# Optimization experiments

Measured on AMD Instinct MI355X. Metric: run time of the kernel, lower is better.

## Reference

```python
import jax, jax.numpy as jnp
import numpy as np


def setup_inputs() -> dict:
    key = jax.random.key(0)
    ks = iter(jax.random.split(key, 100))
    V3, Vm, K, E3, Em = 100000, 25000, 128, 800000, 200000
    c_in, c3, cm, c_out = 16, 128, 256, 21
    rn = lambda *s: jax.random.normal(next(ks), s, dtype=jnp.float32)
    ru = lambda *s: jax.random.uniform(next(ks), s, dtype=jnp.float32)
    ri = lambda hi, *s: jax.random.randint(next(ks), s, 0, hi)
    d = {}
    d['x_in'] = rn(1, V3, c_in)
    d['mass_3'] = ru(1, V3)
    d['evals_3'] = ru(1, K)
    d['evecs_3'] = rn(1, V3, K) * 0.01
    d['gX3_idx'] = ri(V3, E3, 2)
    d['gX3_val'] = rn(E3) * 0.05
    d['gY3_idx'] = ri(V3, E3, 2)
    d['gY3_val'] = rn(E3) * 0.05
    d['mass_m'] = ru(1, Vm)
    d['evals_m'] = ru(1, K)
    d['evecs_m'] = rn(1, Vm, K) * 0.01
    d['gXm_idx'] = ri(Vm, Em, 2)
    d['gXm_val'] = rn(Em) * 0.05
    d['gYm_idx'] = ri(Vm, Em, 2)
    d['gYm_val'] = rn(Em) * 0.05
    d['traces34'] = ri(Vm, V3)
    d['in_w'] = rn(c_in, c3) * 0.05
    d['in_b'] = rn(c3) * 0.05
    d['widen_w'] = rn(c3, cm) * 0.05
    d['widen_b'] = rn(cm) * 0.05
    d['narrow_w'] = rn(cm, c3) * 0.05
    d['narrow_b'] = rn(c3) * 0.05
    d['halve_w'] = rn(2 * c3, c3) * 0.05
    d['halve_b'] = rn(c3) * 0.05
    d['out_w'] = rn(c3, c_out) * 0.05
    d['out_b'] = rn(c_out) * 0.05
    for pre, C in (('enc', c3), ('mid', cm), ('dec', c3)):
        d[pre + '_dt'] = ru(2, C)
        d[pre + '_Are'] = rn(2, C, C) * 0.05
        d[pre + '_Aim'] = rn(2, C, C) * 0.05
        d[pre + '_w0'] = rn(2, 3 * C, C) * 0.05
        d[pre + '_b0'] = rn(2, C) * 0.05
        d[pre + '_w1'] = rn(2, C, C) * 0.05
        d[pre + '_b1'] = rn(2, C) * 0.05
        d[pre + '_w2'] = rn(2, C, C) * 0.05
        d[pre + '_b2'] = rn(2, C) * 0.05
    return d


def _spmm(idx, val, x, n):
    # sparse COO (n x n) @ x ; rows = idx[:,0], cols = idx[:,1]
    return jax.ops.segment_sum(val[:, None] * x[idx[:, 1]], idx[:, 0], num_segments=n)


def _block(x, mass, evals, evecs, gxi, gxv, gyi, gyv, dt, Are, Aim, w0, b0, w1, b1, w2, b2):
    # DiffusionNetBlock: spectral diffusion + rotated gradient features + MiniMLP + residual
    V = x.shape[1]
    x_spec = jnp.einsum('bvk,bvc->bkc', evecs, x * mass[..., None])          # to_basis
    coef = jnp.exp(-evals[..., None] * jnp.maximum(dt, 1e-8)[None, None, :])  # (B,K,C)
    xd = jnp.einsum('bvk,bkc->bvc', evecs, coef * x_spec)                     # from_basis
    gX = _spmm(gxi, gxv, xd[0], V)[None]                                      # (B,V,C)
    gY = _spmm(gyi, gyv, xd[0], V)[None]
    Br = gX @ Are - gY @ Aim                                                  # complex linear, with rotations
    Bi = gY @ Are + gX @ Aim
    gf = jnp.tanh(gX * Br + gY * Bi)                                          # inner product -> tanh
    h = jnp.concatenate([x, xd, gf], axis=-1)                                 # (B,V,3C)
    h = jax.nn.relu(h @ w0 + b0)
    h = jax.nn.relu(h @ w1 + b1)
    return (h @ w2 + b2) + x


def reference(x_in, mass_3, evals_3, evecs_3, gX3_idx, gX3_val, gY3_idx, gY3_val,
              mass_m, evals_m, evecs_m, gXm_idx, gXm_val, gYm_idx, gYm_val, traces34,
              in_w, in_b, enc_dt, enc_Are, enc_Aim, enc_w0, enc_b0, enc_w1, enc_b1, enc_w2, enc_b2,
              widen_w, widen_b, mid_dt, mid_Are, mid_Aim, mid_w0, mid_b0, mid_w1, mid_b1, mid_w2, mid_b2,
              narrow_w, narrow_b, halve_w, halve_b,
              dec_dt, dec_Are, dec_Aim, dec_w0, dec_b0, dec_w1, dec_b1, dec_w2, dec_b2,
              out_w, out_b):
    Vm = mass_m.shape[1]
    sl = lambda arrs, i: tuple(a[i] for a in arrs)
    enc_p = (enc_dt, enc_Are, enc_Aim, enc_w0, enc_b0, enc_w1, enc_b1, enc_w2, enc_b2)
    mid_p = (mid_dt, mid_Are, mid_Aim, mid_w0, mid_b0, mid_w1, mid_b1, mid_w2, mid_b2)
    dec_p = (dec_dt, dec_Are, dec_Aim, dec_w0, dec_b0, dec_w1, dec_b1, dec_w2, dec_b2)

    x3 = jax.nn.relu(x_in @ in_w + in_b)
    for i in range(enc_dt.shape[0]):
        x3 = _block(x3, mass_3, evals_3, evecs_3, gX3_idx, gX3_val, gY3_idx, gY3_val, *sl(enc_p, i))
    # scatter-max pooling fine -> coarse
    xm = jax.ops.segment_max(x3[0], traces34, num_segments=Vm)
    xm = jnp.where(jnp.isneginf(xm), 0.0, xm)[None]
    xm = jax.nn.relu(xm @ widen_w + widen_b)
    for i in range(mid_dt.shape[0]):
        xm = _block(xm, mass_m, evals_m, evecs_m, gXm_idx, gXm_val, gYm_idx, gYm_val, *sl(mid_p, i))
    # gather unpooling coarse -> fine
    y3 = xm[:, traces34, :]
    y3 = jax.nn.relu(y3 @ narrow_w + narrow_b)
    y3 = jnp.concatenate([y3, x3], axis=-1)
    y3 = jax.nn.relu(y3 @ halve_w + halve_b)
    for i in range(dec_dt.shape[0]):
        y3 = _block(y3, mass_3, evals_3, evecs_3, gX3_idx, gX3_val, gY3_idx, gY3_val, *sl(dec_p, i))
    return y3 @ out_w + out_b
```

## Files before the change

### kernel.cpp

```cpp
#include <hip/hip_runtime.h>
#include <cstdint>
#include <cstddef>

static constexpr int V3   = 100000;
static constexpr int VM   = 25000;
static constexpr int KE   = 128;
static constexpr int E3   = 800000;
static constexpr int EM   = 200000;
static constexpr int C3   = 128;
static constexpr int CMID = 256;

typedef unsigned short u16;
typedef unsigned int   u32;
using short8v = __attribute__((ext_vector_type(8))) short;
using f32x4   = __attribute__((ext_vector_type(4))) float;
using f32x16  = __attribute__((ext_vector_type(16))) float;

#define DEVI __device__ __forceinline__
DEVI float4 ld4(const float* p){ return *(const float4*)p; }
DEVI void   st4(float* p, float4 v){ *(float4*)p = v; }
DEVI float  bf2f(u16 u){ return __uint_as_float(((u32)u) << 16); }
DEVI u16    f2bf(float f){
  u32 u = __float_as_uint(f);
  u += 0x7FFFu + ((u >> 16) & 1u);
  return (u16)(u >> 16);
}
DEVI u32 pk2(float a, float b){ return (u32)f2bf(a) | ((u32)f2bf(b) << 16); }
DEVI short8v as8(uint4 v){ union { uint4 u; short8v s; } c; c.u = v; return c.s; }
DEVI int lofs(int row, int oct){ return row * 40 + ((oct ^ ((row >> 3) & 3)) << 3); }

static inline int cdiv(int a, int b){ return (a + b - 1) / b; }

template<bool RELU, bool RES, bool GATHER, bool OBF16>
__global__ __launch_bounds__(256)
void k_mgemm(const void* __restrict__ A0, int aty0, int K0,
             const u16* __restrict__ wt0, int wl0, int wo0,
             const void* __restrict__ A1, int aty1, int K1,
             const u16* __restrict__ wt1, int wl1, int wo1,
             const void* __restrict__ A2, int aty2, int K2,
             const u16* __restrict__ wt2, int wl2, int wo2,
             const int* __restrict__ gidx,
             const float* __restrict__ bias, const float* __restrict__ res,
             void* __restrict__ OUT, u16* __restrict__ OUTB, int CO, int V)
{
  __shared__ __align__(16) u16 As[64 * 40];
  __shared__ __align__(16) u16 Ws[128 * 40];

  const int tid  = threadIdx.x;
  const int wave = tid >> 6, lane = tid & 63;
  const int vbase = blockIdx.x * 64;
  const int ncol0 = blockIdx.y * 128;
  const int KT = K0 + K1 + K2;

  f32x4 acc[8];
  #pragma unroll
  for (int n = 0; n < 8; n++) { acc[n][0]=0.f; acc[n][1]=0.f; acc[n][2]=0.f; acc[n][3]=0.f; }

  const int ar = tid >> 2, ac = tid & 3;
  const int arow = vbase + ar;
  int grow0 = arow;
  if (GATHER && arow < V) grow0 = gidx[arow];

  for (int kt = 0; kt < KT; kt += 32) {
    {
      int kg = kt + ac * 8;
      uint4 aw = make_uint4(0,0,0,0);
      if (arow < V && kg < KT) {
        const void* src; int aty, koff, sK; bool s0;
        if (kg < K0)            { src=A0; aty=aty0; koff=0;     sK=K0; s0=true;  }
        else if (kg < K0 + K1)  { src=A1; aty=aty1; koff=K0;    sK=K1; s0=false; }
        else                    { src=A2; aty=aty2; koff=K0+K1; sK=K2; s0=false; }
        int row = (GATHER && s0) ? grow0 : arow;
        int kl = kg - koff;
        if (aty) {
          aw = *(const uint4*)((const u16*)src + (size_t)row * sK + kl);
        } else {
          const float* fp = (const float*)src + (size_t)row * sK + kl;
          float4 x = ld4(fp), y = ld4(fp + 4);
          aw = make_uint4(pk2(x.x,x.y), pk2(x.z,x.w), pk2(y.x,y.y), pk2(y.z,y.w));
        }
      }
      *(uint4*)&As[ar * 40 + ac * 8] = aw;
    }
    #pragma unroll
    for (int i = 0; i < 2; i++) {
      int col = tid & 127;
      int c = (tid >> 7) + 2 * i;
      int kg = kt + c * 8;
      uint4 ww = make_uint4(0,0,0,0);
      if (kg < KT) {
        const u16* wt; int koff, wl, wo;
        if (kg < K0)           { wt=wt0; koff=0;     wl=wl0; wo=wo0; }
        else if (kg < K0+K1)   { wt=wt1; koff=K0;    wl=wl1; wo=wo1; }
        else                   { wt=wt2; koff=K0+K1; wl=wl2; wo=wo2; }
        ww = *(const uint4*)(wt + (size_t)(ncol0 + col) * wl + wo + (kg - koff));
      }
      *(uint4*)&Ws[col * 40 + c * 8] = ww;
    }
    __syncthreads();
    {
      const int mrow = (wave << 4) + (lane & 15);
      const int kc = lane >> 4;
      short8v a = *(const short8v*)(const void*)&As[mrow * 40 + kc * 8];
      #pragma unroll
      for (int n = 0; n < 8; n++) {
        short8v b = *(const short8v*)(const void*)&Ws[(n * 16 + (lane & 15)) * 40 + kc * 8];
        acc[n] = __builtin_amdgcn_mfma_f32_16x16x32_bf16(a, b, acc[n], 0, 0, 0);
      }
    }
    __syncthreads();
  }

  const int q4 = (lane >> 4) * 4, colb = lane & 15;
  #pragma unroll
  for (int n = 0; n < 8; n++) {
    int gcol = ncol0 + n * 16 + colb;
    float bv = bias ? bias[gcol] : 0.f;
    #pragma unroll
    for (int q = 0; q < 4; q++) {
      int grow = vbase + (wave << 4) + q4 + q;
      if (grow >= V) continue;
      float o = acc[n][q] + bv;
      size_t idx = (size_t)grow * CO + gcol;
      if (RES) o += res[idx];
      if (RELU) o = fmaxf(o, 0.f);
      if (OBF16) ((u16*)OUT)[idx] = f2bf(o);
      else {
        ((float*)OUT)[idx] = o;
        if (OUTB) OUTB[idx] = f2bf(o);
      }
    }
  }
}

__global__ __launch_bounds__(256)
void k_mlp3(const u16* __restrict__ A0, const u16* __restrict__ A1,
            const u16* __restrict__ A2,
            const u16* __restrict__ w0t,
            const u16* __restrict__ w1t, const u16* __restrict__ w2t,
            const float* __restrict__ b0, const float* __restrict__ b1,
            const float* __restrict__ b2,
            float* __restrict__ XM, u16* __restrict__ SHB, int V)
{
  __shared__ __align__(16) u16 As[64 * 40];
  __shared__ __align__(16) u16 Ws[128 * 40];
  __shared__ __align__(16) u16 Hs[4][64 * 40];

  const int tid  = threadIdx.x;
  const int wave = tid >> 6, lane = tid & 63;
  const int vbase = blockIdx.x * 64;
  const int ar = tid >> 2, ac = tid & 3;
  const int arow = vbase + ar;
  const bool rok = arow < V;
  const int mrow = (wave << 4) + (lane & 15);
  const int kc = lane >> 4;
  const int q4 = (lane >> 4) * 4, colb = lane & 15;
  const int wcol = tid & 127, wc = tid >> 7;

  float xres[8][4];
  #pragma unroll
  for (int n = 0; n < 8; n++)
    #pragma unroll
    for (int q = 0; q < 4; q++) {
      int grow = vbase + (wave << 4) + q4 + q;
      xres[n][q] = (grow < V) ? XM[(size_t)grow * C3 + n * 16 + colb] : 0.f;
    }

  f32x4 acc[8];
  auto zacc = [&]{
    #pragma unroll
    for (int n = 0; n < 8; n++) { acc[n][0]=0.f; acc[n][1]=0.f; acc[n][2]=0.f; acc[n][3]=0.f; }
  };
  auto hwrite = [&](const float* b){
    #pragma unroll
    for (int n = 0; n < 8; n++) {
      int c = n * 16 + colb;
      float bv = b[c];
      #pragma unroll
      for (int q = 0; q < 4; q++) {
        int row = (wave << 4) + q4 + q;
        Hs[c >> 5][lofs(row, (c >> 3) & 3) + (c & 7)] = f2bf(fmaxf(acc[n][q] + bv, 0.f));
      }
    }
  };
  auto mfma_tile = [&](const u16* a8){
    short8v a = *(const short8v*)(const void*)a8;
    #pragma unroll
    for (int n = 0; n < 8; n++) {
      short8v b = *(const short8v*)(const void*)&Ws[(n * 16 + (lane & 15)) * 40 + kc * 8];
      acc[n] = __builtin_amdgcn_mfma_f32_16x16x32_bf16(a, b, acc[n], 0, 0, 0);
    }
  };
  auto fA = [&](int kg) -> uint4 {
    const u16* src = (kg < 128) ? A0 : (kg < 256) ? A1 : A2;
    uint4 r = make_uint4(0,0,0,0);
    if (rok) r = *(const uint4*)(src + (size_t)arow * 128 + (kg & 127));
    return r;
  };
  auto fW = [&](const u16* wt, int ld, int kg) -> uint4 {
    return *(const uint4*)(wt + (size_t)wcol * ld + kg);
  };

  zacc();
  uint4 pa  = fA(ac * 8);
  uint4 pw0 = fW(w0t, 384, wc * 8);
  uint4 pw1 = fW(w0t, 384, (wc + 2) * 8);
  for (int kt = 0; kt < 384; kt += 32) {
    __syncthreads();
    *(uint4*)&As[ar * 40 + ac * 8] = pa;
    *(uint4*)&Ws[wcol * 40 + wc * 8] = pw0;
    *(uint4*)&Ws[wcol * 40 + (wc + 2) * 8] = pw1;
    __syncthreads();
    int kn = kt + 32;
    if (kn < 384) {
      pa  = fA(kn + ac * 8);
      pw0 = fW(w0t, 384, kn + wc * 8);
      pw1 = fW(w0t, 384, kn + (wc + 2) * 8);
    } else {
      pw0 = fW(w1t, 128, wc * 8);
      pw1 = fW(w1t, 128, (wc + 2) * 8);
    }
    mfma_tile(&As[mrow * 40 + kc * 8]);
  }
  hwrite(b0);
  zacc();
  for (int kt = 0; kt < 128; kt += 32) {
    __syncthreads();
    *(uint4*)&Ws[wcol * 40 + wc * 8] = pw0;
    *(uint4*)&Ws[wcol * 40 + (wc + 2) * 8] = pw1;
    __syncthreads();
    int kn = kt + 32;
    if (kn < 128) {
      pw0 = fW(w1t, 128, kn + wc * 8);
      pw1 = fW(w1t, 128, kn + (wc + 2) * 8);
    } else {
      pw0 = fW(w2t, 128, wc * 8);
      pw1 = fW(w2t, 128, (wc + 2) * 8);
    }
    mfma_tile(&Hs[kt >> 5][lofs(mrow, kc)]);
  }
  hwrite(b1);
  zacc();
  for (int kt = 0; kt < 128; kt += 32) {
    __syncthreads();
    *(uint4*)&Ws[wcol * 40 + wc * 8] = pw0;
    *(uint4*)&Ws[wcol * 40 + (wc + 2) * 8] = pw1;
    __syncthreads();
    int kn = kt + 32;
    if (kn < 128) {
      pw0 = fW(w2t, 128, kn + wc * 8);
      pw1 = fW(w2t, 128, kn + (wc + 2) * 8);
    }
    mfma_tile(&Hs[kt >> 5][lofs(mrow, kc)]);
  }
  #pragma unroll
  for (int n = 0; n < 8; n++) {
    int gcol = n * 16 + colb;
    float bv = b2[gcol];
    #pragma unroll
    for (int q = 0; q < 4; q++) {
      int grow = vbase + (wave << 4) + q4 + q;
      if (grow >= V) continue;
      size_t idx = (size_t)grow * C3 + gcol;
      float o = acc[n][q] + bv + xres[n][q];
      XM[idx] = o;
      SHB[idx] = f2bf(o);
    }
  }
}

__global__ __launch_bounds__(256)
void k_mgate_reg(const u16* __restrict__ GEX, const u16* __restrict__ GEY,
                 const u16* __restrict__ pS, const u16* __restrict__ pR,
                 const u16* __restrict__ pI,
                 u16* __restrict__ GF, int CO, int V)
{
  const int lane = threadIdx.x & 63;
  const int wave = threadIdx.x >> 6;
  const int rbase = blockIdx.x * 128 + wave * 32;
  const int arow = rbase + (lane & 31);
  const int koff = (lane >> 5) * 8;
  const bool rok = arow < V;

  uint4 ax[8], ay[8], an[8];
  #pragma unroll
  for (int kt = 0; kt < 8; kt++) {
    uint4 zx = make_uint4(0,0,0,0), zy = make_uint4(0,0,0,0);
    if (rok) {
      zx = *(const uint4*)(GEX + (size_t)arow * KE + kt * 16 + koff);
      zy = *(const uint4*)(GEY + (size_t)arow * KE + kt * 16 + koff);
    }
    ax[kt] = zx; ay[kt] = zy;
    an[kt] = make_uint4(zy.x ^ 0x80008000u, zy.y ^ 0x80008000u,
                        zy.z ^ 0x80008000u, zy.w ^ 0x80008000u);
  }

  const int ngr = CO >> 5;
  for (int g = 0; g < ngr; g++) {
    f32x16 gx, gy, br, bi;
    #pragma unroll
    for (int r = 0; r < 16; r++) { gx[r]=0.f; gy[r]=0.f; br[r]=0.f; bi[r]=0.f; }
    #pragma unroll
    for (int kt = 0; kt < 8; kt++) {
      size_t bo = ((size_t)(g * 8 + kt) * 64 + lane) * 8;
      short8v bs  = *(const short8v*)(const void*)(pS + bo);
      short8v brv = *(const short8v*)(const void*)(pR + bo);
      short8v biv = *(const short8v*)(const void*)(pI + bo);
      short8v axv = as8(ax[kt]), ayv = as8(ay[kt]), anv = as8(an[kt]);
      gx = __builtin_amdgcn_mfma_f32_32x32x16_bf16(axv, bs,  gx, 0, 0, 0);
      gy = __builtin_amdgcn_mfma_f32_32x32x16_bf16(ayv, bs,  gy, 0, 0, 0);
      br = __builtin_amdgcn_mfma_f32_32x32x16_bf16(axv, brv, br, 0, 0, 0);
      br = __builtin_amdgcn_mfma_f32_32x32x16_bf16(anv, biv, br, 0, 0, 0);
      bi = __builtin_amdgcn_mfma_f32_32x32x16_bf16(axv, biv, bi, 0, 0, 0);
      bi = __builtin_amdgcn_mfma_f32_32x32x16_bf16(ayv, brv, bi, 0, 0, 0);
    }
    const int col = g * 32 + (lane & 31);
    const int rhi = 4 * (lane >> 5);
    #pragma unroll
    for (int r = 0; r < 16; r++) {
      int row = rbase + (r & 3) + 8 * (r >> 2) + rhi;
      if (row < V) {
        float o = tanhf(gx[r] * br[r] + gy[r] * bi[r]);
        GF[(size_t)row * CO + col] = f2bf(o);
      }
    }
  }
}

__global__ __launch_bounds__(256)
void k_specmm(const u16* __restrict__ E, const u16* __restrict__ X,
              const float* __restrict__ mass, float* __restrict__ SPEC,
              int C, int V, int CH)
{
  __shared__ __align__(16) u16 As[64 * 40];
  __shared__ __align__(16) u16 Bs[128 * 40];

  const int tid = threadIdx.x;
  const int wave = tid >> 6, lane = tid & 63;
  const int m0 = blockIdx.y * 64;
  const int n0 = blockIdx.z * 128;
  const int vs = blockIdx.x * CH;
  const int ve = min(V, vs + CH);

  f32x4 acc[8];
  #pragma unroll
  for (int n = 0; n < 8; n++) { acc[n][0]=0.f; acc[n][1]=0.f; acc[n][2]=0.f; acc[n][3]=0.f; }

  const int am = tid & 63, ac = tid >> 6;
  const int bcol = tid & 127, bc0 = (tid >> 7) * 2;

  u16 ea[8]; float fb0[8], fb1[8], fm0[8], fm1[8];
  auto loadA = [&](int kt) {
    #pragma unroll
    for (int j = 0; j < 8; j++) {
      int v = kt + ac * 8 + j;
      ea[j] = (v < ve) ? E[(size_t)v * KE + m0 + am] : (u16)0;
    }
  };
  auto loadB = [&](int kt) {
    #pragma unroll
    for (int j = 0; j < 8; j++) {
      int v0 = kt + bc0 * 8 + j, v1 = v0 + 8;
      fb0[j] = (v0 < ve) ? bf2f(X[(size_t)v0 * C + n0 + bcol]) : 0.f;
      fm0[j] = (v0 < ve) ? mass[v0] : 0.f;
      fb1[j] = (v1 < ve) ? bf2f(X[(size_t)v1 * C + n0 + bcol]) : 0.f;
      fm1[j] = (v1 < ve) ? mass[v1] : 0.f;
    }
  };
  loadA(vs); loadB(vs);

  for (int kt = vs; kt < ve; kt += 32) {
    __syncthreads();
    *(uint4*)&As[lofs(am, ac)] = make_uint4(
        (u32)ea[0] | ((u32)ea[1] << 16), (u32)ea[2] | ((u32)ea[3] << 16),
        (u32)ea[4] | ((u32)ea[5] << 16), (u32)ea[6] | ((u32)ea[7] << 16));
    float t0[8], t1[8];
    #pragma unroll
    for (int j = 0; j < 8; j++) { t0[j] = fb0[j]*fm0[j]; t1[j] = fb1[j]*fm1[j]; }
    *(uint4*)&Bs[lofs(bcol, bc0)] = make_uint4(
        pk2(t0[0],t0[1]), pk2(t0[2],t0[3]), pk2(t0[4],t0[5]), pk2(t0[6],t0[7]));
    *(uint4*)&Bs[lofs(bcol, bc0 + 1)] = make_uint4(
        pk2(t1[0],t1[1]), pk2(t1[2],t1[3]), pk2(t1[4],t1[5]), pk2(t1[6],t1[7]));
    __syncthreads();
    if (kt + 32 < ve) { loadA(kt + 32); loadB(kt + 32); }
    const int kc = lane >> 4, ml = lane & 15;
    short8v a = *(const short8v*)(const void*)&As[lofs(wave * 16 + ml, kc)];
    #pragma unroll
    for (int n = 0; n < 8; n++) {
      short8v b = *(const short8v*)(const void*)&Bs[lofs(n * 16 + ml, kc)];
      acc[n] = __builtin_amdgcn_mfma_f32_16x16x32_bf16(a, b, acc[n], 0, 0, 0);
    }
  }

  const int q4 = (lane >> 4) * 4, colb = lane & 15;
  #pragma unroll
  for (int n = 0; n < 8; n++) {
    int col = n0 + n * 16 + colb;
    #pragma unroll
    for (int q = 0; q < 4; q++) {
      int row = m0 + wave * 16 + q4 + q;
      unsafeAtomicAdd(&SPEC[(size_t)row * C + col], acc[n][q]);
    }
  }
}

template<int C>
__global__ void k_smallprep(const float* __restrict__ SPEC, const float* __restrict__ evals,
                            const float* __restrict__ dt, const float* __restrict__ Are,
                            const float* __restrict__ Aim, const float* __restrict__ w0,
                            u16* __restrict__ pS, u16* __restrict__ pR,
                            u16* __restrict__ pI, u16* __restrict__ SWt)
{
  __shared__ float sld[C];
  const int k = blockIdx.x;
  const int c = threadIdx.x;
  const float ev = evals[k];
  float s = expf(-ev * fmaxf(dt[c], 1e-8f)) * SPEC[(size_t)k * C + c];
  sld[c] = s;
  const size_t pidx = ((size_t)((c >> 5) * 8 + (k >> 4)) * 64
                       + (c & 31) + ((k >> 3) & 1) * 32) * 8 + (k & 7);
  pS[pidx] = f2bf(s);
  __syncthreads();
  float tr = 0.f, ti = 0.f, sw = 0.f;
  for (int j = 0; j < C; j++) {
    float sj = sld[j];
    tr = fmaf(sj, Are[(size_t)j * C + c], tr);
    ti = fmaf(sj, Aim[(size_t)j * C + c], ti);
    sw = fmaf(sj, w0[(size_t)(C + j) * C + c], sw);
  }
  pR[pidx] = f2bf(tr);
  pI[pidx] = f2bf(ti);
  SWt[(size_t)c * 128 + k] = f2bf(sw);
}

__global__ void k_asmw0(const u16* __restrict__ w0t_, const u16* __restrict__ swt_,
                        u16* __restrict__ o_) {
  int col = blockIdx.x, t = threadIdx.x;
  o_[(size_t)col * 384 + t]       = w0t_[(size_t)col * 384 + t];
  o_[(size_t)col * 384 + 128 + t] = w0t_[(size_t)col * 384 + 256 + t];
  o_[(size_t)col * 384 + 256 + t] = swt_[(size_t)col * 128 + t];
}

__global__ void k_prepw(const float* __restrict__ W, u16* __restrict__ WT, int K, int N) {
  size_t zoff = (size_t)blockIdx.z * K * N;
  int i = blockIdx.x * 256 + threadIdx.x;
  if (i < K * N) {
    int k = i / N, n = i % N;
    WT[zoff + (size_t)n * K + k] = f2bf(W[zoff + i]);
  }
}

__global__ void k_cvt(const float* __restrict__ in, u16* __restrict__ out, int n) {
  int i = (blockIdx.x * 256 + threadIdx.x) * 4;
  if (i < n) {
    float4 v = ld4(in + i);
    ushort4 o; o.x = f2bf(v.x); o.y = f2bf(v.y); o.z = f2bf(v.z); o.w = f2bf(v.w);
    *(ushort4*)(out + i) = o;
  }
}

__global__ void k_hist(const int* __restrict__ idx, int* __restrict__ deg, int E) {
  int e = blockIdx.x * 256 + threadIdx.x;
  if (e < E) atomicAdd(&deg[idx[2 * e]], 1);
}
__global__ void k_scan1(const int* __restrict__ deg, int* __restrict__ excl,
                        int* __restrict__ bsum, int V) {
  __shared__ int sd[256];
  int t = threadIdx.x;
  int i = blockIdx.x * 256 + t;
  int v = (i < V) ? deg[i] : 0;
  sd[t] = v;
  __syncthreads();
  for (int off = 1; off < 256; off <<= 1) {
    int add = (t >= off) ? sd[t - off] : 0;
    __syncthreads();
    sd[t] += add;
    __syncthreads();
  }
  if (i < V) excl[i] = sd[t] - v;
  if (t == 255) bsum[blockIdx.x] = sd[255];
}
__global__ void k_scan2(int* __restrict__ bsum, int nb, int* __restrict__ rowptr, int V) {
  __shared__ int sd[512];
  int t = threadIdx.x;
  int v = (t < nb) ? bsum[t] : 0;
  sd[t] = v;
  __syncthreads();
  for (int off = 1; off < 512; off <<= 1) {
    int add = (t >= off) ? sd[t - off] : 0;
    __syncthreads();
    sd[t] += add;
    __syncthreads();
  }
  if (t < nb) bsum[t] = sd[t] - v;
  if (t == 0) rowptr[V] = sd[511];
}
__global__ void k_scan3(const int* __restrict__ excl, const int* __restrict__ bsum,
                        int* __restrict__ rowptr, int V) {
  int i = blockIdx.x * 256 + threadIdx.x;
  if (i < V) rowptr[i] = excl[i] + bsum[i >> 8];
}
__global__ void k_scatter(const int* __restrict__ idx, const float* __restrict__ val,
                          const int* __restrict__ rowptr, int* __restrict__ cur,
                          int* __restrict__ ecol, float* __restrict__ eval, int E) {
  int e = blockIdx.x * 256 + threadIdx.x;
  if (e < E) {
    int d = idx[2 * e];
    int p = rowptr[d] + atomicAdd(&cur[d], 1);
    ecol[p] = idx[2 * e + 1];
    eval[p] = val[e];
  }
}
__global__ __launch_bounds__(256)
void k_spmm_csr(const int* __restrict__ rowptr, const int* __restrict__ ecol,
                const float* __restrict__ eval, const u16* __restrict__ E,
                u16* __restrict__ GE, int V) {
  int r = blockIdx.x * 8 + (threadIdx.x >> 5);
  int lane = threadIdx.x & 31;
  if (r >= V) return;
  int j1 = rowptr[r + 1];
  float4 a = make_float4(0.f,0.f,0.f,0.f);
  for (int j = rowptr[r]; j < j1; j++) {
    int c = ecol[j];
    float v = eval[j];
    ushort4 x = *(const ushort4*)(E + (size_t)c * KE + lane * 4);
    a.x = fmaf(v, bf2f(x.x), a.x); a.y = fmaf(v, bf2f(x.y), a.y);
    a.z = fmaf(v, bf2f(x.z), a.z); a.w = fmaf(v, bf2f(x.w), a.w);
  }
  ushort4 o;
  o.x = f2bf(a.x); o.y = f2bf(a.y); o.z = f2bf(a.z); o.w = f2bf(a.w);
  *(ushort4*)(GE + (size_t)r * KE + lane * 4) = o;
}

__global__ void k_segmax_init(unsigned* __restrict__ u, int n) {
  int i = blockIdx.x * 256 + threadIdx.x;
  if (i < n) u[i] = 0x007FFFFFu;
}
__global__ void k_segmax_scatter(const u16* __restrict__ X, const int* __restrict__ tr,
                                 unsigned* __restrict__ u) {
  int i = blockIdx.x * 256 + threadIdx.x;
  if (i >= V3 * C3) return;
  int v = i >> 7, c = i & 127;
  unsigned b = ((unsigned)X[i]) << 16;
  unsigned m = (b & 0x80000000u) ? ~b : (b | 0x80000000u);
  atomicMax(&u[((size_t)tr[v] << 7) + c], m);
}
__global__ void k_segmax_decode(const unsigned* __restrict__ u, u16* __restrict__ out, int n) {
  int i = blockIdx.x * 256 + threadIdx.x;
  if (i < n) {
    unsigned m = u[i];
    unsigned b = 0;
    if (m != 0x007FFFFFu)
      b = (m & 0x80000000u) ? (m & 0x7FFFFFFFu) : ~m;
    out[i] = (u16)(b >> 16);
  }
}

__global__ __launch_bounds__(256)
void k_outproj(const float* __restrict__ Y, const float* __restrict__ W,
               const float* __restrict__ B, float* __restrict__ OUT, int V) {
  __shared__ float Wl[128][22];
  __shared__ float ys[8][128];
  const int tid = threadIdx.x;
  for (int f = tid; f < 128 * 21; f += 256) Wl[f / 21][f % 21] = W[f];
  {
    int r = tid >> 5, cc = (tid & 31) * 4;
    int v = blockIdx.x * 8 + r;
    float4 yv = make_float4(0.f,0.f,0.f,0.f);
    if (v < V) yv = ld4(Y + (size_t)v * C3 + cc);
    st4(&ys[r][cc], yv);
  }
  __syncthreads();
  int r = tid >> 5, c = tid & 31;
  int v = blockIdx.x * 8 + r;
  if (v < V && c < 21) {
    float acc = B[c];
    #pragma unroll 8
    for (int k = 0; k < 128; k++) acc = fmaf(ys[r][k], Wl[k][c], acc);
    OUT[(size_t)v * 21 + c] = acc;
  }
}

extern "C" void kernel_launch(void* const* d_in, const int* in_sizes, int n_in,
                              void* d_out, int out_size, void* d_ws, size_t ws_size,
                              hipStream_t stream)
{
  (void)in_sizes; (void)n_in; (void)out_size;
  const float* x_in    = (const float*)d_in[0];
  const float* mass3   = (const float*)d_in[1];
  const float* evals3  = (const float*)d_in[2];
  const float* evecs3  = (const float*)d_in[3];
  const int*   gX3i    = (const int*)d_in[4];
  const float* gX3v    = (const float*)d_in[5];
  const int*   gY3i    = (const int*)d_in[6];
  const float* gY3v    = (const float*)d_in[7];
  const float* massm   = (const float*)d_in[8];
  const float* evalsm  = (const float*)d_in[9];
  const float* evecsm  = (const float*)d_in[10];
  const int*   gXmi    = (const int*)d_in[11];
  const float* gXmv    = (const float*)d_in[12];
  const int*   gYmi    = (const int*)d_in[13];
  const float* gYmv    = (const float*)d_in[14];
  const int*   tr34    = (const int*)d_in[15];
  const float* in_w    = (const float*)d_in[16];
  const float* in_b    = (const float*)d_in[17];
  const float* widen_w = (const float*)d_in[18];
  const float* widen_b = (const float*)d_in[19];
  const float* narrow_w= (const float*)d_in[20];
  const float* narrow_b= (const float*)d_in[21];
  const float* halve_w = (const float*)d_in[22];
  const float* halve_b = (const float*)d_in[23];
  const float* out_w   = (const float*)d_in[24];
  const float* out_b   = (const float*)d_in[25];
  const float* enc_p[9]; const float* mid_p[9]; const float* dec_p[9];
  for (int i = 0; i < 9; i++) {
    enc_p[i] = (const float*)d_in[26 + i];
    mid_p[i] = (const float*)d_in[35 + i];
    dec_p[i] = (const float*)d_in[44 + i];
  }

  char* ws = (char*)d_ws;
  size_t off = 0;
  float* XM  = (float*)(ws + off); off += (size_t)V3 * C3 * 4;
  u16* SHB   = (u16*)(ws + off);   off += (size_t)V3 * C3 * 2;
  u16* GEX3  = (u16*)(ws + off);   off += (size_t)V3 * KE * 2;
  u16* GEY3  = (u16*)(ws + off);   off += (size_t)V3 * KE * 2;
  u16* GEXm  = (u16*)(ws + off);   off += (size_t)VM * KE * 2;
  u16* GEYm  = (u16*)(ws + off);   off += (size_t)VM * KE * 2;
  u16* BSCR  = (u16*)(ws + off);   off += (size_t)V3 * C3 * 2;
  char* E3R  = (char*)(ws + off);  off += (size_t)V3 * KE * 2;
  u16* Embf  = (u16*)(ws + off);   off += (size_t)VM * KE * 2;
  u16* SHM   = (u16*)(ws + off);   off += (size_t)VM * CMID * 2;
  float* spec= (float*)(ws + off); off += 131072;
  u16* pS  = (u16*)(ws + off); off += 65536;
  u16* pR  = (u16*)(ws + off); off += 65536;
  u16* pI  = (u16*)(ws + off); off += 65536;
  u16* SWt = (u16*)(ws + off); off += 65536;
  u16* wT  = (u16*)(ws + off); off += 2400000;
  const size_t NEED = off;
  if (ws_size < NEED) return;

  u16*   E3bf = (u16*)E3R;
  float* M0   = (float*)E3R;
  int*   rowptr = (int*)BSCR;
  int*   deg    = (int*)((char*)BSCR + 400128);
  int*   ecol   = (int*)((char*)BSCR + 800256);
  float* evalv  = (float*)((char*)BSCR + 4000256);
  int*   bsum   = (int*)((char*)BSCR + 7200256);
  unsigned* xm_u  = (unsigned*)BSCR;
  u16*      xm_dec= (u16*)((char*)BSCR + 12800000);
  u16* BSCR0 = BSCR;
  u16* BSCR1 = BSCR + (size_t)VM * CMID;

  u16* in_wt    = wT + 0;
  u16* widen_t  = wT + 2048;
  u16* narrow_t = wT + 34816;
  u16* halve_t  = wT + 67584;
  u16* enc_w0t  = wT + 100352;
  u16* enc_w1t  = wT + 198656;
  u16* enc_w2t  = wT + 231424;
  u16* mid_w0t  = wT + 264192;
  u16* mid_w1t  = wT + 657408;
  u16* mid_w2t  = wT + 788480;
  u16* dec_w0t  = wT + 919552;
  u16* dec_w1t  = wT + 1017856;
  u16* dec_w2t  = wT + 1050624;
  u16* wCmb     = wT + 1083392;

  auto prepw = [&](const float* W, u16* WT, int K, int N, int z) {
    k_prepw<<<dim3(cdiv(K * N, 256), 1, z), 256, 0, stream>>>(W, WT, K, N);
  };
  prepw(in_w, in_wt, 16, 128, 1);
  prepw(widen_w, widen_t, 128, 256, 1);
  prepw(narrow_w, narrow_t, 256, 128, 1);
  prepw(halve_w, halve_t, 256, 128, 1);
  prepw(enc_p[3], enc_w0t, 384, 128, 2);
  prepw(enc_p[5], enc_w1t, 128, 128, 2);
  prepw(enc_p[7], enc_w2t, 128, 128, 2);
  prepw(mid_p[3], mid_w0t, 768, 256, 2);
  prepw(mid_p[5], mid_w1t, 256, 256, 2);
  prepw(mid_p[7], mid_w2t, 256, 256, 2);
  prepw(dec_p[3], dec_w0t, 384, 128, 2);
  prepw(dec_p[5], dec_w1t, 128, 128, 2);
  prepw(dec_p[7], dec_w2t, 128, 128, 2);

  k_cvt<<<cdiv(V3 * KE / 4, 256), 256, 0, stream>>>(evecs3, E3bf, V3 * KE);
  k_cvt<<<cdiv(VM * KE / 4, 256), 256, 0, stream>>>(evecsm, Embf, VM * KE);

  auto build_ge = [&](const int* idx, const float* val, int E_, int V_,
                      const u16* Ebf, u16* GE) {
    hipMemsetAsync(deg, 0, (size_t)V_ * 4, stream);
    k_hist<<<cdiv(E_, 256), 256, 0, stream>>>(idx, deg, E_);
    int nb = cdiv(V_, 256);
    k_scan1<<<nb, 256, 0, stream>>>(deg, ecol, bsum, V_);
    k_scan2<<<1, 512, 0, stream>>>(bsum, nb, rowptr, V_);
    k_scan3<<<nb, 256, 0, stream>>>(ecol, bsum, rowptr, V_);
    hipMemsetAsync(deg, 0, (size_t)V_ * 4, stream);
    k_scatter<<<cdiv(E_, 256), 256, 0, stream>>>(idx, val, rowptr, deg, ecol, evalv, E_);
    k_spmm_csr<<<cdiv(V_, 8), 256, 0, stream>>>(rowptr, ecol, evalv, Ebf, GE, V_);
  };
  build_ge(gX3i, gX3v, E3, V3, E3bf, GEX3);
  build_ge(gY3i, gY3v, E3, V3, E3bf, GEY3);
  build_ge(gXmi, gXmv, EM, VM, Embf, GEXm);
  build_ge(gYmi, gYmv, EM, VM, Embf, GEYm);

  const int G3 = cdiv(V3, 64);
  const int GM = cdiv(VM, 64);

  auto launch_block3 = [&](const float* p[9],
                           const u16* w0t, const u16* w1t, const u16* w2t, int i) {
    const float* dt  = p[0] + (size_t)i * C3;
    const float* Are = p[1] + (size_t)i * C3 * C3;
    const float* Aim = p[2] + (size_t)i * C3 * C3;
    const float* w0  = p[3] + (size_t)i * 3 * C3 * C3;
    const float* b0  = p[4] + (size_t)i * C3;
    const float* b1  = p[6] + (size_t)i * C3;
    const float* b2  = p[8] + (size_t)i * C3;
    const u16* w0ti = w0t + (size_t)i * 3 * C3 * C3;
    const u16* w1ti = w1t + (size_t)i * C3 * C3;
    const u16* w2ti = w2t + (size_t)i * C3 * C3;
    hipMemsetAsync(spec, 0, (size_t)KE * C3 * 4, stream);
    k_specmm<<<dim3(cdiv(V3, 256), 2, 1), 256, 0, stream>>>(E3bf, SHB, mass3, spec, C3, V3, 256);
    k_smallprep<C3><<<KE, C3, 0, stream>>>(spec, evals3, dt, Are, Aim, w0, pS, pR, pI, SWt);
    k_mgate_reg<<<cdiv(V3, 128), 256, 0, stream>>>(GEX3, GEY3, pS, pR, pI, BSCR, C3, V3);
    k_asmw0<<<128, 128, 0, stream>>>(w0ti, SWt, wCmb);
    k_mlp3<<<G3, 256, 0, stream>>>(SHB, BSCR, E3bf, wCmb, w1ti, w2ti,
                                   b0, b1, b2, XM, SHB, V3);
  };

  auto run_blockm = [&](const float* p[9],
                        const u16* w0t, const u16* w1t, const u16* w2t, int i) {
    const float* dt  = p[0] + (size_t)i * CMID;
    const float* Are = p[1] + (size_t)i * CMID * CMID;
    const float* Aim = p[2] + (size_t)i * CMID * CMID;
    const float* w0  = p[3] + (size_t)i * 3 * CMID * CMID;
    const float* b0  = p[4] + (size_t)i * CMID;
    const float* b1  = p[6] + (size_t)i * CMID;
    const float* b2  = p[8] + (size_t)i * CMID;
    const u16* w0ti = w0t + (size_t)i * 3 * CMID * CMID;
    const u16* w1ti = w1t + (size_t)i * CMID * CMID;
    const u16* w2ti = w2t + (size_t)i * CMID * CMID;
    hipMemsetAsync(spec, 0, (size_t)KE * CMID * 4, stream);
    k_specmm<<<dim3(cdiv(VM, 128), 2, 2), 256, 0, stream>>>(Embf, SHM, massm, spec, CMID, VM, 128);
    k_smallprep<CMID><<<KE, CMID, 0, stream>>>(spec, evalsm, dt, Are, Aim, w0, pS, pR, pI, SWt);
    k_mgate_reg<<<cdiv(VM, 128), 256, 0, stream>>>(GEXm, GEYm, pS, pR, pI, BSCR0, CMID, VM);
    k_mgemm<true,false,false,true><<<dim3(GM, 2), 256, 0, stream>>>(
        SHM, 1, CMID, w0ti, 3*CMID, 0,
        BSCR0, 1, CMID, w0ti, 3*CMID, 2*CMID,
        Embf, 1, KE, SWt, 128, 0,
        nullptr, b0, nullptr, BSCR1, nullptr, CMID, VM);
    k_mgemm<true,false,false,true><<<dim3(GM, 2), 256, 0, stream>>>(
        BSCR1, 1, CMID, w1ti, CMID, 0,
        nullptr,0,0,nullptr,0,0, nullptr,0,0,nullptr,0,0,
        nullptr, b1, nullptr, BSCR0, nullptr, CMID, VM);
    k_mgemm<false,true,false,false><<<dim3(GM, 2), 256, 0, stream>>>(
        BSCR0, 1, CMID, w2ti, CMID, 0,
        nullptr,0,0,nullptr,0,0, nullptr,0,0,nullptr,0,0,
        nullptr, b2, M0, M0, SHM, CMID, VM);
  };

  k_mgemm<true,false,false,false><<<dim3(G3, 1), 256, 0, stream>>>(
      x_in, 0, 16, in_wt, 16, 0,
      nullptr,0,0,nullptr,0,0, nullptr,0,0,nullptr,0,0,
      nullptr, in_b, nullptr, XM, SHB, C3, V3);
  launch_block3(enc_p, enc_w0t, enc_w1t, enc_w2t, 0);
  launch_block3(enc_p, enc_w0t, enc_w1t, enc_w2t, 1);

  k_segmax_init<<<cdiv(VM * C3, 256), 256, 0, stream>>>(xm_u, VM * C3);
  k_segmax_scatter<<<cdiv(V3 * C3, 256), 256, 0, stream>>>(SHB, tr34, xm_u);
  k_segmax_decode<<<cdiv(VM * C3, 256), 256, 0, stream>>>(xm_u, xm_dec, VM * C3);
  k_mgemm<true,false,false,false><<<dim3(GM, 2), 256, 0, stream>>>(
      xm_dec, 1, C3, widen_t, C3, 0,
      nullptr,0,0,nullptr,0,0, nullptr,0,0,nullptr,0,0,
      nullptr, widen_b, nullptr, M0, SHM, CMID, VM);
  run_blockm(mid_p, mid_w0t, mid_w1t, mid_w2t, 0);
  run_blockm(mid_p, mid_w0t, mid_w1t, mid_w2t, 1);

  k_mgemm<true,false,true,true><<<dim3(G3, 1), 256, 0, stream>>>(
      SHM, 1, CMID, narrow_t, CMID, 0,
      nullptr,0,0,nullptr,0,0, nullptr,0,0,nullptr,0,0,
      tr34, narrow_b, nullptr, BSCR, nullptr, C3, V3);
  k_mgemm<true,false,false,false><<<dim3(G3, 1), 256, 0, stream>>>(
      BSCR, 1, C3, halve_t, 2*C3, 0,
      SHB, 1, C3, halve_t, 2*C3, C3,
      nullptr,0,0,nullptr,0,0,
      nullptr, halve_b, nullptr, XM, SHB, C3, V3);

  k_cvt<<<cdiv(V3 * KE / 4, 256), 256, 0, stream>>>(evecs3, E3bf, V3 * KE);
  launch_block3(dec_p, dec_w0t, dec_w1t, dec_w2t, 0);
  launch_block3(dec_p, dec_w0t, dec_w1t, dec_w2t, 1);

  k_outproj<<<cdiv(V3, 8), 256, 0, stream>>>(XM, out_w, out_b, (float*)d_out, V3);
}
```

Before: 2.005 ms.

## Pre-pack MLP weights into MFMA fragment order and drop LDS staging

```diff
diff --git a/kernel.cpp b/kernel.cpp
--- a/kernel.cpp
+++ b/kernel.cpp
@@ -134,37 +134,24 @@
 }
 
 __global__ __launch_bounds__(256)
-void k_mlp3(const u16* __restrict__ A0, const u16* __restrict__ A1,
-            const u16* __restrict__ A2,
-            const u16* __restrict__ w0t,
-            const u16* __restrict__ w1t, const u16* __restrict__ w2t,
-            const float* __restrict__ b0, const float* __restrict__ b1,
-            const float* __restrict__ b2,
-            float* __restrict__ XM, u16* __restrict__ SHB, int V)
+void k_mlp3r(const u16* __restrict__ A0, const u16* __restrict__ A1,
+             const u16* __restrict__ A2,
+             const u16* __restrict__ w0p,
+             const u16* __restrict__ w1p, const u16* __restrict__ w2p,
+             const float* __restrict__ b0, const float* __restrict__ b1,
+             const float* __restrict__ b2,
+             float* __restrict__ XM, u16* __restrict__ SHB, int V)
 {
-  __shared__ __align__(16) u16 As[64 * 40];
-  __shared__ __align__(16) u16 Ws[128 * 40];
   __shared__ __align__(16) u16 Hs[4][64 * 40];
 
   const int tid  = threadIdx.x;
   const int wave = tid >> 6, lane = tid & 63;
   const int vbase = blockIdx.x * 64;
-  const int ar = tid >> 2, ac = tid & 3;
-  const int arow = vbase + ar;
+  const int colb = lane & 15;
+  const int q4 = (lane >> 4) * 4;
+  const int kq = (lane >> 4) * 8;
+  const int arow = vbase + wave * 16 + colb;
   const bool rok = arow < V;
-  const int mrow = (wave << 4) + (lane & 15);
-  const int kc = lane >> 4;
-  const int q4 = (lane >> 4) * 4, colb = lane & 15;
-  const int wcol = tid & 127, wc = tid >> 7;
-
-  float xres[8][4];
-  #pragma unroll
-  for (int n = 0; n < 8; n++)
-    #pragma unroll
-    for (int q = 0; q < 4; q++) {
-      int grow = vbase + (wave << 4) + q4 + q;
-      xres[n][q] = (grow < V) ? XM[(size_t)grow * C3 + n * 16 + colb] : 0.f;
-    }
 
   f32x4 acc[8];
   auto zacc = [&]{
@@ -183,75 +170,41 @@
       }
     }
   };
-  auto mfma_tile = [&](const u16* a8){
-    short8v a = *(const short8v*)(const void*)a8;
+
+  zacc();
+  #pragma unroll
+  for (int kc = 0; kc < 12; kc++) {
+    int kg = kc * 32 + kq;
+    const u16* src = (kg < 128) ? A0 : (kg < 256) ? A1 : A2;
+    short8v a = as8(make_uint4(0,0,0,0));
+    if (rok) a = *(const short8v*)(const void*)(src + (size_t)arow * 128 + (kg & 127));
     #pragma unroll
     for (int n = 0; n < 8; n++) {
-      short8v b = *(const short8v*)(const void*)&Ws[(n * 16 + (lane & 15)) * 40 + kc * 8];
+      short8v b = *(const short8v*)(const void*)(w0p + ((size_t)(n * 12 + kc) * 64 + lane) * 8);
       acc[n] = __builtin_amdgcn_mfma_f32_16x16x32_bf16(a, b, acc[n], 0, 0, 0);
     }
-  };
-  auto fA = [&](int kg) -> uint4 {
-    const u16* src = (kg < 128) ? A0 : (kg < 256) ? A1 : A2;
-    uint4 r = make_uint4(0,0,0,0);
-    if (rok) r = *(const uint4*)(src + (size_t)arow * 128 + (kg & 127));
-    return r;
-  };
-  auto fW = [&](const u16* wt, int ld, int kg) -> uint4 {
-    return *(const uint4*)(wt + (size_t)wcol * ld + kg);
-  };
-
-  zacc();
-  uint4 pa  = fA(ac * 8);
-  uint4 pw0 = fW(w0t, 384, wc * 8);
-  uint4 pw1 = fW(w0t, 384, (wc + 2) * 8);
-  for (int kt = 0; kt < 384; kt += 32) {
-    __syncthreads();
-    *(uint4*)&As[ar * 40 + ac * 8] = pa;
-    *(uint4*)&Ws[wcol * 40 + wc * 8] = pw0;
-    *(uint4*)&Ws[wcol * 40 + (wc + 2) * 8] = pw1;
-    __syncthreads();
-    int kn = kt + 32;
-    if (kn < 384) {
-      pa  = fA(kn + ac * 8);
-      pw0 = fW(w0t, 384, kn + wc * 8);
-      pw1 = fW(w0t, 384, kn + (wc + 2) * 8);
-    } else {
-      pw0 = fW(w1t, 128, wc * 8);
-      pw1 = fW(w1t, 128, (wc + 2) * 8);
-    }
-    mfma_tile(&As[mrow * 40 + kc * 8]);
   }
   hwrite(b0);
   zacc();
-  for (int kt = 0; kt < 128; kt += 32) {
-    __syncthreads();
-    *(uint4*)&Ws[wcol * 40 + wc * 8] = pw0;
-    *(uint4*)&Ws[wcol * 40 + (wc + 2) * 8] = pw1;
-    __syncthreads();
-    int kn = kt + 32;
-    if (kn < 128) {
-      pw0 = fW(w1t, 128, kn + wc * 8);
-      pw1 = fW(w1t, 128, kn + (wc + 2) * 8);
-    } else {
-      pw0 = fW(w2t, 128, wc * 8);
-      pw1 = fW(w2t, 128, (wc + 2) * 8);
-    }
-    mfma_tile(&Hs[kt >> 5][lofs(mrow, kc)]);
+  #pragma unroll
+  for (int kc = 0; kc < 4; kc++) {
+    short8v a = *(const short8v*)(const void*)&Hs[kc][lofs((wave << 4) + colb, lane >> 4)];
+    #pragma unroll
+    for (int n = 0; n < 8; n++) {
+      short8v b = *(const short8v*)(const void*)(w1p + ((size_t)(n * 4 + kc) * 64 + lane) * 8);
+      acc[n] = __builtin_amdgcn_mfma_f32_16x16x32_bf16(a, b, acc[n], 0, 0, 0);
+    }
   }
   hwrite(b1);
   zacc();
-  for (int kt = 0; kt < 128; kt += 32) {
-    __syncthreads();
-    *(uint4*)&Ws[wcol * 40 + wc * 8] = pw0;
-    *(uint4*)&Ws[wcol * 40 + (wc + 2) * 8] = pw1;
-    __syncthreads();
-    int kn = kt + 32;
-    if (kn < 128) {
-      pw0 = fW(w2t, 128, kn + wc * 8);
-      pw1 = fW(w2t, 128, kn + (wc + 2) * 8);
-    }
-    mfma_tile(&Hs[kt >> 5][lofs(mrow, kc)]);
+  #pragma unroll
+  for (int kc = 0; kc < 4; kc++) {
+    short8v a = *(const short8v*)(const void*)&Hs[kc][lofs((wave << 4) + colb, lane >> 4)];
+    #pragma unroll
+    for (int n = 0; n < 8; n++) {
+      short8v b = *(const short8v*)(const void*)(w2p + ((size_t)(n * 4 + kc) * 64 + lane) * 8);
+      acc[n] = __builtin_amdgcn_mfma_f32_16x16x32_bf16(a, b, acc[n], 0, 0, 0);
+    }
   }
   #pragma unroll
   for (int n = 0; n < 8; n++) {
@@ -262,11 +215,38 @@
       int grow = vbase + (wave << 4) + q4 + q;
       if (grow >= V) continue;
       size_t idx = (size_t)grow * C3 + gcol;
-      float o = acc[n][q] + bv + xres[n][q];
+      float o = acc[n][q] + bv + XM[idx];
       XM[idx] = o;
       SHB[idx] = f2bf(o);
     }
   }
+}
+
+__global__ void k_packw(const u16* __restrict__ wt, u16* __restrict__ dst, int K) {
+  int NKC = K >> 5;
+  int gid = blockIdx.x * 256 + threadIdx.x;
+  if (gid >= 8 * NKC * 64) return;
+  int lane = gid & 63, t = gid >> 6;
+  int kc = t % NKC, n = t / NKC;
+  int col = n * 16 + (lane & 15);
+  int k0 = kc * 32 + ((lane >> 4) * 8);
+  uint4 w = *(const uint4*)(wt + (size_t)col * K + k0);
+  *(uint4*)(dst + (size_t)gid * 8) = w;
+}
+__global__ void k_packw0(const u16* __restrict__ w0t, const u16* __restrict__ swt,
+                         u16* __restrict__ dst) {
+  int gid = blockIdx.x * 256 + threadIdx.x;
+  if (gid >= 8 * 12 * 64) return;
+  int lane = gid & 63, t = gid >> 6;
+  int kc = t % 12, n = t / 12;
+  int col = n * 16 + (lane & 15);
+  int k0 = kc * 32 + ((lane >> 4) * 8);
+  const u16* s; size_t o;
+  if (k0 < 128)      { s = w0t; o = (size_t)col * 384 + k0; }
+  else if (k0 < 256) { s = w0t; o = (size_t)col * 384 + k0 + 128; }
+  else               { s = swt; o = (size_t)col * 128 + (k0 - 256); }
+  uint4 w = *(const uint4*)(s + o);
+  *(uint4*)(dst + (size_t)gid * 8) = w;
 }
 
 __global__ __launch_bounds__(256)
@@ -431,14 +411,6 @@
   pR[pidx] = f2bf(tr);
   pI[pidx] = f2bf(ti);
   SWt[(size_t)c * 128 + k] = f2bf(sw);
-}
-
-__global__ void k_asmw0(const u16* __restrict__ w0t_, const u16* __restrict__ swt_,
-                        u16* __restrict__ o_) {
-  int col = blockIdx.x, t = threadIdx.x;
-  o_[(size_t)col * 384 + t]       = w0t_[(size_t)col * 384 + t];
-  o_[(size_t)col * 384 + 128 + t] = w0t_[(size_t)col * 384 + 256 + t];
-  o_[(size_t)col * 384 + 256 + t] = swt_[(size_t)col * 128 + t];
 }
 
 __global__ void k_prepw(const float* __restrict__ W, u16* __restrict__ WT, int K, int N) {
@@ -636,7 +608,7 @@
   u16* pR  = (u16*)(ws + off); off += 65536;
   u16* pI  = (u16*)(ws + off); off += 65536;
   u16* SWt = (u16*)(ws + off); off += 65536;
-  u16* wT  = (u16*)(ws + off); off += 2400000;
+  u16* wT  = (u16*)(ws + off); off += 2800000;
   const size_t NEED = off;
   if (ws_size < NEED) return;
 
@@ -665,7 +637,8 @@
   u16* dec_w0t  = wT + 919552;
   u16* dec_w1t  = wT + 1017856;
   u16* dec_w2t  = wT + 1050624;
-  u16* wCmb     = wT + 1083392;
+  u16* w0p      = wT + 1083392;
+  u16* wpk      = wT + 1150016;
 
   auto prepw = [&](const float* W, u16* WT, int K, int N, int z) {
     k_prepw<<<dim3(cdiv(K * N, 256), 1, z), 256, 0, stream>>>(W, WT, K, N);
@@ -684,6 +657,17 @@
   prepw(dec_p[5], dec_w1t, 128, 128, 2);
   prepw(dec_p[7], dec_w2t, 128, 128, 2);
 
+  u16* enc_w1p[2] = { wpk + 0,      wpk + 16384 };
+  u16* enc_w2p[2] = { wpk + 32768,  wpk + 49152 };
+  u16* dec_w1p[2] = { wpk + 65536,  wpk + 81920 };
+  u16* dec_w2p[2] = { wpk + 98304,  wpk + 114688 };
+  for (int i = 0; i < 2; i++) {
+    k_packw<<<8, 256, 0, stream>>>(enc_w1t + (size_t)i * C3 * C3, enc_w1p[i], 128);
+    k_packw<<<8, 256, 0, stream>>>(enc_w2t + (size_t)i * C3 * C3, enc_w2p[i], 128);
+    k_packw<<<8, 256, 0, stream>>>(dec_w1t + (size_t)i * C3 * C3, dec_w1p[i], 128);
+    k_packw<<<8, 256, 0, stream>>>(dec_w2t + (size_t)i * C3 * C3, dec_w2p[i], 128);
+  }
+
   k_cvt<<<cdiv(V3 * KE / 4, 256), 256, 0, stream>>>(evecs3, E3bf, V3 * KE);
   k_cvt<<<cdiv(VM * KE / 4, 256), 256, 0, stream>>>(evecsm, Embf, VM * KE);
 
@@ -707,8 +691,8 @@
   const int G3 = cdiv(V3, 64);
   const int GM = cdiv(VM, 64);
 
-  auto launch_block3 = [&](const float* p[9],
-                           const u16* w0t, const u16* w1t, const u16* w2t, int i) {
+  auto launch_block3 = [&](const float* p[9], const u16* w0t,
+                           const u16* w1p_, const u16* w2p_, int i) {
     const float* dt  = p[0] + (size_t)i * C3;
     const float* Are = p[1] + (size_t)i * C3 * C3;
     const float* Aim = p[2] + (size_t)i * C3 * C3;
@@ -717,15 +701,13 @@
     const float* b1  = p[6] + (size_t)i * C3;
     const float* b2  = p[8] + (size_t)i * C3;
     const u16* w0ti = w0t + (size_t)i * 3 * C3 * C3;
-    const u16* w1ti = w1t + (size_t)i * C3 * C3;
-    const u16* w2ti = w2t + (size_t)i * C3 * C3;
     hipMemsetAsync(spec, 0, (size_t)KE * C3 * 4, stream);
     k_specmm<<<dim3(cdiv(V3, 256), 2, 1), 256, 0, stream>>>(E3bf, SHB, mass3, spec, C3, V3, 256);
     k_smallprep<C3><<<KE, C3, 0, stream>>>(spec, evals3, dt, Are, Aim, w0, pS, pR, pI, SWt);
     k_mgate_reg<<<cdiv(V3, 128), 256, 0, stream>>>(GEX3, GEY3, pS, pR, pI, BSCR, C3, V3);
-    k_asmw0<<<128, 128, 0, stream>>>(w0ti, SWt, wCmb);
-    k_mlp3<<<G3, 256, 0, stream>>>(SHB, BSCR, E3bf, wCmb, w1ti, w2ti,
-                                   b0, b1, b2, XM, SHB, V3);
+    k_packw0<<<24, 256, 0, stream>>>(w0ti, SWt, w0p);
+    k_mlp3r<<<G3, 256, 0, stream>>>(SHB, BSCR, E3bf, w0p, w1p_, w2p_,
+                                    b0, b1, b2, XM, SHB, V3);
   };
 
   auto run_blockm = [&](const float* p[9],
@@ -763,8 +745,8 @@
       x_in, 0, 16, in_wt, 16, 0,
       nullptr,0,0,nullptr,0,0, nullptr,0,0,nullptr,0,0,
       nullptr, in_b, nullptr, XM, SHB, C3, V3);
-  launch_block3(enc_p, enc_w0t, enc_w1t, enc_w2t, 0);
-  launch_block3(enc_p, enc_w0t, enc_w1t, enc_w2t, 1);
+  launch_block3(enc_p, enc_w0t, enc_w1p[0], enc_w2p[0], 0);
+  launch_block3(enc_p, enc_w0t, enc_w1p[1], enc_w2p[1], 1);
 
   k_segmax_init<<<cdiv(VM * C3, 256), 256, 0, stream>>>(xm_u, VM * C3);
   k_segmax_scatter<<<cdiv(V3 * C3, 256), 256, 0, stream>>>(SHB, tr34, xm_u);
@@ -787,8 +769,8 @@
       nullptr, halve_b, nullptr, XM, SHB, C3, V3);
 
   k_cvt<<<cdiv(V3 * KE / 4, 256), 256, 0, stream>>>(evecs3, E3bf, V3 * KE);
-  launch_block3(dec_p, dec_w0t, dec_w1t, dec_w2t, 0);
-  launch_block3(dec_p, dec_w0t, dec_w1t, dec_w2t, 1);
+  launch_block3(dec_p, dec_w0t, dec_w1p[0], dec_w2p[0], 0);
+  launch_block3(dec_p, dec_w0t, dec_w1p[1], dec_w2p[1], 1);
 
   k_outproj<<<cdiv(V3, 8), 256, 0, stream>>>(XM, out_w, out_b, (float*)d_out, V3);
 }
```

Result: no change. 1.985 ms (-1.0%).
